# Kernel tuning notes

Measured on AMD Instinct MI355X. Metric: run time of the kernel, lower is better.

Reference implementation:

```python
import jax, jax.numpy as jnp
import numpy as np

NUM_E = 50000
EMBED_DIM = 128
HID_DIM = 200
B = 512
N = 50  # candidate_num / history length
ITER_NUM = 3
ALPHA = 0.5
WEIGHT_BASE = 1.0
SQUASH_W = 1.0
SQUASH_EPS = 1e-9
L2_EPS = 1e-12  # torch F.normalize default eps


def setup_inputs() -> dict:
    key = jax.random.key(0)
    k1, k2, k3, k4, k5, k6, k7 = jax.random.split(key, 7)
    idx = jax.random.randint(k1, (B, N), 0, NUM_E)
    times = jax.random.randint(k2, (B, N), 0, 365)
    # embeddings: normal then row-wise L2 normalize (as in init_embeddings)
    emb = jax.random.normal(k3, (NUM_E, EMBED_DIM), dtype=jnp.float32)
    embeddings = emb / jnp.maximum(jnp.linalg.norm(emb, axis=1, keepdims=True), L2_EPS)
    Ws_w = jax.random.normal(k4, (HID_DIM, EMBED_DIM), dtype=jnp.float32) * (2.0 / (HID_DIM + EMBED_DIM)) ** 0.5
    Ws_b = jnp.zeros((HID_DIM,), dtype=jnp.float32)
    mlp_w = jax.random.normal(k5, (NUM_E, HID_DIM), dtype=jnp.float32) * (2.0 / (NUM_E + HID_DIM)) ** 0.5
    mlp_b = jnp.zeros((NUM_E,), dtype=jnp.float32)
    return {"idx": idx, "times": times, "embeddings": embeddings,
            "Ws_w": Ws_w, "Ws_b": Ws_b, "mlp_w": mlp_w, "mlp_b": mlp_b}


def _squash(s):
    # s: [B, H]; squash over last axis (original axis=-2 on [B,1,1,H,1])
    sq = jnp.sum(s * s, axis=-1, keepdims=True)
    scale = sq / (SQUASH_W + sq) / jnp.sqrt(sq + SQUASH_EPS)
    return scale * s


def reference(idx, times, embeddings, Ws_w, Ws_b, mlp_w, mlp_b):
    # gather history embeddings: [B, N, D]
    embeds = embeddings[idx]
    # temporal weighting -> initial routing logits b_ij: [B, N]
    b = (WEIGHT_BASE + 1.0) / (WEIGHT_BASE + times.astype(jnp.float32))
    # Ws linear (dropout is identity at eval): [B, N, H]
    x = jnp.einsum('bnd,hd->bnh', embeds, Ws_w) + Ws_b
    # u_hat: L2-normalized over H
    u_hat = x / jnp.maximum(jnp.linalg.norm(x, axis=-1, keepdims=True), L2_EPS)
    u_det = jax.lax.stop_gradient(u_hat)
    # dynamic routing, fixed ITER_NUM iterations
    for r in range(ITER_NUM):
        c = jax.nn.softmax(b, axis=1) * N            # [B, N]
        s = jnp.einsum('bn,bnh->bh', c, u_hat)       # [B, H]
        v = _squash(s)                               # [B, H]
        if r < ITER_NUM - 1:
            b = b + jnp.einsum('bnh,bh->bn', u_det, v)
    poses, c_ij = v, c                               # [B, H], [B, N]
    # p_ij: scatter-add c_ij per entity id (math of one_hot^T @ c_ij)
    p = jnp.zeros((B, NUM_E), dtype=jnp.float32)
    p = p.at[jnp.arange(B)[:, None], idx].add(c_ij)
    p = jax.nn.softmax(p, axis=1)
    # decoder mlp (reflect=False)
    scores = poses @ mlp_w.T + mlp_b                 # [B, NUM_E]
    sims = jax.nn.softmax(scores, axis=1)
    return jnp.log(ALPHA * p + (1.0 - ALPHA) * sims)
```

## Files before the change

kernel.cpp:

```cpp
#include <hip/hip_runtime.h>
#include <stdint.h>

#define NUM_E 50000
#define EMBED_DIM 128
#define HID_DIM 200
#define BATCH 512
#define NN 50
#define KPAD 224
#define NKT 7
#define NTT2 3136
#define NXB 196
#define PACK_UNITS 784
#define USTRIDE 201

typedef short s16x8 __attribute__((ext_vector_type(8)));
typedef float f32x4 __attribute__((ext_vector_type(4)));

__device__ inline unsigned short f2bf(float f) {
  union { float f; unsigned u; } v; v.f = f;
  unsigned r = v.u + 0x7FFF + ((v.u >> 16) & 1);
  return (unsigned short)(r >> 16);
}
__device__ inline float bf2f(unsigned short b) {
  union { unsigned u; float f; } v; v.u = ((unsigned)b) << 16;
  return v.f;
}

__device__ __forceinline__ void gl_lds16(const unsigned short* g, unsigned short* l) {
  __builtin_amdgcn_global_load_lds(
      (const __attribute__((address_space(1))) unsigned int*)g,
      (__attribute__((address_space(3))) unsigned int*)l, 16, 0, 0);
}

template<int PASS>
__device__ __forceinline__ void gemm_tile(
    int yb, int xb, char* buf, int tid,
    const unsigned short* Ap, const unsigned short* Bp, const float* mlp_b,
    const float* D_ws, float* S_ws, float* out)
{
  unsigned short* Bs = (unsigned short*)buf;
  float* red = (float*)(buf + 16384);
  const int w = tid >> 6, lane = tid & 63;
  const int q = lane >> 4, l15 = lane & 15;
  const int mt0 = yb * 4;
  const int m0 = yb * 64;
  const int ntb = xb * 16 + w * 4;

  if (PASS == 1 && tid < 64) {
    red[tid]      = 0.5f / D_ws[m0 + tid];
    red[64 + tid] = 0.5f / S_ws[m0 + tid];
  }
  float bias[4];
  #pragma unroll
  for (int nl = 0; nl < 4; ++nl) {
    const int col = (ntb + nl) * 16 + l15;
    bias[nl] = (col < NUM_E) ? mlp_b[col] : 0.f;
  }
  const unsigned short* apBase = Ap + (size_t)mt0 * NKT * 512;

  f32x4 acc[4][4];
  #pragma unroll
  for (int i = 0; i < 4; i++)
    #pragma unroll
    for (int j = 0; j < 4; j++) acc[i][j] = (f32x4){0, 0, 0, 0};

  for (int kt = 0; kt < NKT; ++kt) {
    #pragma unroll
    for (int nl = 0; nl < 4; ++nl)
      gl_lds16(Bp + ((size_t)(ntb + nl) * NKT + kt) * 512 + lane * 8,
               &Bs[(w * 4 + nl) * 512]);
    s16x8 a[4];
    #pragma unroll
    for (int mi = 0; mi < 4; ++mi)
      a[mi] = *(const s16x8*)&apBase[((mi * NKT + kt) * 64 + lane) * 8];
    __syncthreads();
    s16x8 bfr[4];
    #pragma unroll
    for (int nl = 0; nl < 4; ++nl)
      bfr[nl] = *(const s16x8*)&Bs[((w * 4 + nl) * 64 + lane) * 8];
    #pragma unroll
    for (int nl = 0; nl < 4; ++nl)
      #pragma unroll
      for (int mi = 0; mi < 4; ++mi)
        acc[mi][nl] = __builtin_amdgcn_mfma_f32_16x16x32_bf16(a[mi], bfr[nl], acc[mi][nl], 0, 0, 0);
    __syncthreads();
  }

  if (PASS == 0) {
    float rs[4][4];
    #pragma unroll
    for (int mi = 0; mi < 4; mi++)
      #pragma unroll
      for (int p = 0; p < 4; p++) rs[mi][p] = 0.f;
    #pragma unroll
    for (int mi = 0; mi < 4; ++mi)
      #pragma unroll
      for (int nl = 0; nl < 4; ++nl) {
        const int col = (ntb + nl) * 16 + l15;
        #pragma unroll
        for (int p = 0; p < 4; p++) {
          const float v = acc[mi][nl][p] + bias[nl];
          rs[mi][p] += (col < NUM_E) ? __expf(v) : 0.f;
        }
      }
    #pragma unroll
    for (int m = 1; m < 16; m <<= 1)
      for (int mi = 0; mi < 4; mi++)
        for (int p = 0; p < 4; p++)
          rs[mi][p] += __shfl_xor(rs[mi][p], m, 64);
    if (l15 == 0)
      for (int mi = 0; mi < 4; mi++)
        for (int p = 0; p < 4; p++)
          red[w * 64 + mi * 16 + q * 4 + p] = rs[mi][p];
    __syncthreads();
    if (tid < 64)
      atomicAdd(&S_ws[m0 + tid],
                red[tid] + red[64 + tid] + red[128 + tid] + red[192 + tid]);
  } else {
    #pragma unroll
    for (int mi = 0; mi < 4; ++mi) {
      #pragma unroll
      for (int p = 0; p < 4; p++) {
        const int rl = mi * 16 + q * 4 + p;
        const float invD = red[rl];
        const float invS = red[64 + rl];
        const int row = m0 + rl;
        #pragma unroll
        for (int nl = 0; nl < 4; ++nl) {
          const int col = (ntb + nl) * 16 + l15;
          if (col < NUM_E) {
            const float v = acc[mi][nl][p] + bias[nl];
            out[(size_t)row * NUM_E + col] = __logf(fmaf(__expf(v), invS, invD));
          }
        }
      }
    }
  }
}

__global__ __launch_bounds__(256, 3) void k_stage1(
    const int* __restrict__ idx, const int* __restrict__ times,
    const float* __restrict__ emb, const float* __restrict__ Ws_w,
    const float* __restrict__ Ws_b, const float* __restrict__ mlp_w,
    unsigned short* __restrict__ Bp, unsigned short* __restrict__ Ap,
    float* __restrict__ poses_f, float* __restrict__ expa_ws,
    float* __restrict__ D_ws, float* __restrict__ S_ws)
{
  __shared__ __align__(16) char buf[40320];
  __shared__ float cc[NN], bb[NN], vv[HID_DIM], red4[4], scaleS;
  __shared__ int sidx[NN];
  const int u = blockIdx.x;
  const int tid = threadIdx.x;
  const int w = tid >> 6, lane = tid & 63;
  const int q = lane >> 4, l15 = lane & 15;

  if (u < BATCH) {
    const int b = u;
    if (tid < NN) {
      sidx[tid] = idx[b * NN + tid];
      bb[tid] = 2.0f / (1.0f + (float)times[b * NN + tid]);
    }
    __syncthreads();
    unsigned short* Afr = (unsigned short*)buf;
    unsigned short* Bfr = (unsigned short*)(buf + 16384);
    for (int v = tid; v < 1024; v += 256) {
      const int row = v >> 4, c = v & 15;
      const int kt = c >> 2, qq = c & 3;
      unsigned short tmp[8] __attribute__((aligned(16)));
      if (row < NN) {
        const float* src = emb + (size_t)sidx[row] * EMBED_DIM + c * 8;
        float4 f0 = *(const float4*)src;
        float4 f1 = *(const float4*)(src + 4);
        tmp[0] = f2bf(f0.x); tmp[1] = f2bf(f0.y); tmp[2] = f2bf(f0.z); tmp[3] = f2bf(f0.w);
        tmp[4] = f2bf(f1.x); tmp[5] = f2bf(f1.y); tmp[6] = f2bf(f1.z); tmp[7] = f2bf(f1.w);
      } else {
        for (int j = 0; j < 8; j++) tmp[j] = 0;
      }
      *(uint4*)&Afr[(((row >> 4) * 4 + kt) * 64 + qq * 16 + (row & 15)) * 8] = *(uint4*)tmp;
    }
    f32x4 acc[4][4];
    #pragma unroll
    for (int i = 0; i < 4; i++)
      #pragma unroll
      for (int j = 0; j < 4; j++) acc[i][j] = (f32x4){0, 0, 0, 0};
    __syncthreads();
    for (int kt = 0; kt < 4; ++kt) {
      for (int v = tid; v < 832; v += 256) {
        const int n = v >> 2, cq = v & 3;
        unsigned short tmp[8] __attribute__((aligned(16)));
        if (n < HID_DIM) {
          const float* src = Ws_w + (size_t)n * EMBED_DIM + kt * 32 + cq * 8;
          float4 f0 = *(const float4*)src;
          float4 f1 = *(const float4*)(src + 4);
          tmp[0] = f2bf(f0.x); tmp[1] = f2bf(f0.y); tmp[2] = f2bf(f0.z); tmp[3] = f2bf(f0.w);
          tmp[4] = f2bf(f1.x); tmp[5] = f2bf(f1.y); tmp[6] = f2bf(f1.z); tmp[7] = f2bf(f1.w);
        } else {
          for (int j = 0; j < 8; j++) tmp[j] = 0;
        }
        *(uint4*)&Bfr[((n >> 4) * 64 + cq * 16 + (n & 15)) * 8] = *(uint4*)tmp;
      }
      __syncthreads();
      s16x8 a[4];
      #pragma unroll
      for (int mt = 0; mt < 4; ++mt)
        a[mt] = *(const s16x8*)&Afr[((mt * 4 + kt) * 64 + lane) * 8];
      #pragma unroll
      for (int ii = 0; ii < 4; ++ii) {
        const int nt = w + ii * 4;
        if (nt < 13) {
          s16x8 bv = *(const s16x8*)&Bfr[(nt * 64 + lane) * 8];
          #pragma unroll
          for (int mt = 0; mt < 4; ++mt)
            acc[mt][ii] = __builtin_amdgcn_mfma_f32_16x16x32_bf16(a[mt], bv, acc[mt][ii], 0, 0, 0);
        }
      }
      __syncthreads();
    }
    float* uu = (float*)buf;
    #pragma unroll
    for (int ii = 0; ii < 4; ++ii) {
      const int nt = w + ii * 4;
      if (nt < 13) {
        const int col = nt * 16 + l15;
        if (col < HID_DIM) {
          const float bv = Ws_b[col];
          #pragma unroll
          for (int mt = 0; mt < 4; ++mt)
            #pragma unroll
            for (int p = 0; p < 4; p++) {
              const int row = mt * 16 + q * 4 + p;
              if (row < NN) uu[row * USTRIDE + col] = acc[mt][ii][p] + bv;
            }
        }
      }
    }
    __syncthreads();
    const int un = tid >> 2, uc0 = (tid & 3) * 50;
    if (un < NN) {
      float s = 0.f;
      for (int j = 0; j < 50; j++) {
        const float x = uu[un * USTRIDE + uc0 + j];
        s += x * x;
      }
      s += __shfl_xor(s, 1, 64);
      s += __shfl_xor(s, 2, 64);
      const float inv = 1.0f / fmaxf(sqrtf(s), 1e-12f);
      for (int j = 0; j < 50; j++) uu[un * USTRIDE + uc0 + j] *= inv;
    }
    __syncthreads();
    for (int it = 0; it < 3; ++it) {
      if (tid < 64) {
        float x = (tid < NN) ? bb[tid] : -1e30f;
        float m = x;
        for (int d = 1; d < 64; d <<= 1) m = fmaxf(m, __shfl_xor(m, d, 64));
        float e = (tid < NN) ? __expf(x - m) : 0.f;
        float s = e;
        for (int d = 1; d < 64; d <<= 1) s += __shfl_xor(s, d, 64);
        if (tid < NN) cc[tid] = e * (float)NN / s;
      }
      __syncthreads();
      float sh = 0.f;
      if (tid < HID_DIM)
        for (int n = 0; n < NN; n++) sh += cc[n] * uu[n * USTRIDE + tid];
      float sq2 = (tid < HID_DIM) ? sh * sh : 0.f;
      for (int d = 1; d < 64; d <<= 1) sq2 += __shfl_xor(sq2, d, 64);
      if ((tid & 63) == 0) red4[tid >> 6] = sq2;
      __syncthreads();
      if (tid == 0) {
        const float t2 = red4[0] + red4[1] + red4[2] + red4[3];
        scaleS = t2 / (1.0f + t2) / sqrtf(t2 + 1e-9f);
      }
      __syncthreads();
      if (tid < HID_DIM) vv[tid] = scaleS * sh;
      __syncthreads();
      if (it < 2) {
        float d = 0.f;
        if (un < NN)
          for (int j = 0; j < 50; j++)
            d += uu[un * USTRIDE + uc0 + j] * vv[uc0 + j];
        d += __shfl_xor(d, 1, 64);
        d += __shfl_xor(d, 2, 64);
        if (un < NN && (tid & 3) == 0) bb[un] += d;
        __syncthreads();
      }
    }
    if (tid < KPAD) {
      const float val = (tid < HID_DIM) ? vv[tid] : 0.f;
      const int kt = tid >> 5, rem = tid & 31, qq = rem >> 3, j = rem & 7;
      const int mt = b >> 4, ll = b & 15;
      Ap[(size_t)(((mt * NKT + kt) * 64) + qq * 16 + ll) * 8 + j] = f2bf(val);
    }
    if (tid < HID_DIM) poses_f[b * HID_DIM + tid] = vv[tid];
    if (tid < 64) {
      float a2 = 0.f; int first = 1;
      const int my = (tid < NN) ? sidx[tid] : -1;
      if (tid < NN) {
        for (int n = 0; n < NN; n++)
          if (sidx[n] == my) { a2 += cc[n]; if (n < tid) first = 0; }
        expa_ws[b * NN + tid] = __expf(a2);
      }
      float contrib = (tid < NN && first) ? (__expf(a2) - 1.0f) : 0.f;
      for (int d = 1; d < 64; d <<= 1) contrib += __shfl_xor(contrib, d, 64);
      if (tid == 0) D_ws[b] = (float)NUM_E + contrib;
    }
  } else if (u < BATCH + PACK_UNITS) {
    const int pb = u - BATCH;
    unsigned short* smem = (unsigned short*)buf;
    const size_t base_f = (size_t)pb * 64 * HID_DIM;
    const float4* src4 = (const float4*)(mlp_w + base_f);
    for (int i = tid; i < 3200; i += 256) {
      float4 f;
      if (base_f + 4 * (size_t)i + 4 <= (size_t)NUM_E * HID_DIM) f = src4[i];
      else f = make_float4(0.f, 0.f, 0.f, 0.f);
      unsigned short t4[4] __attribute__((aligned(8))) = {
        f2bf(f.x), f2bf(f.y), f2bf(f.z), f2bf(f.w)};
      *(uint2*)&smem[i * 4] = *(uint2*)t4;
    }
    __syncthreads();
    const int nt0 = pb * 4;
    unsigned short* dst = Bp + (size_t)nt0 * NKT * 512;
    for (int s2 = 0; s2 < 7; ++s2) {
      const int fi = s2 * 256 + tid;
      const int fr = fi >> 6;
      const int ln = fi & 63;
      const int nt_l = fr / 7, kt = fr - nt_l * 7;
      const int r = nt_l * 16 + (ln & 15);
      const int kb = kt * 32 + (ln >> 4) * 8;
      uint4 val;
      if (kb < HID_DIM) val = *(const uint4*)&smem[r * HID_DIM + kb];
      else val = make_uint4(0, 0, 0, 0);
      *(uint4*)&dst[(size_t)fi * 8] = val;
    }
  } else {
    S_ws[tid] = 0.f;
    S_ws[256 + tid] = 0.f;
  }
}

template<int PASS>
__global__ __launch_bounds__(256, 4) void k_gemm(
    const unsigned short* __restrict__ Ap, const unsigned short* __restrict__ Bp,
    const float* __restrict__ mlp_b, const float* __restrict__ D_ws,
    float* __restrict__ S_ws, float* __restrict__ out)
{
  __shared__ __align__(16) char buf2[17408];
  const int id = blockIdx.x;
  const int yb = id / 200;
  const int xb = id - yb * 200;
  if (xb >= NXB) return;
  gemm_tile<PASS>(yb, xb, buf2, threadIdx.x, Ap, Bp, mlp_b, D_ws, S_ws, out);
}

__global__ __launch_bounds__(256) void k_fix(
    const int* __restrict__ idx, const float* __restrict__ expa,
    const float* __restrict__ poses_f, const float* __restrict__ mlp_w,
    const float* __restrict__ mlp_b, const float* __restrict__ D_ws,
    const float* __restrict__ S_ws, float* __restrict__ out)
{
  const int t = blockIdx.x * 4 + (threadIdx.x >> 6);
  const int lane = threadIdx.x & 63;
  if (t >= BATCH * NN) return;
  const int b = t / NN;
  const int j = idx[t];
  float dot = 0.f;
  for (int h = lane; h < HID_DIM; h += 64)
    dot += poses_f[b * HID_DIM + h] * mlp_w[(size_t)j * HID_DIM + h];
  for (int m = 1; m < 64; m <<= 1) dot += __shfl_xor(dot, m, 64);
  if (lane == 0) {
    const float s = dot + mlp_b[j];
    out[(size_t)b * NUM_E + j] = __logf(0.5f * expa[t] / D_ws[b] +
                                        0.5f * __expf(s) / S_ws[b]);
  }
}

extern "C" void kernel_launch(void* const* d_in, const int* in_sizes, int n_in,
                              void* d_out, int out_size, void* d_ws, size_t ws_size,
                              hipStream_t stream) {
  const int*   idx   = (const int*)d_in[0];
  const int*   times = (const int*)d_in[1];
  const float* emb   = (const float*)d_in[2];
  const float* Ws_w  = (const float*)d_in[3];
  const float* Ws_b  = (const float*)d_in[4];
  const float* mlp_w = (const float*)d_in[5];
  const float* mlp_b = (const float*)d_in[6];
  float* out = (float*)d_out;

  char* ws = (char*)d_ws;
  unsigned short* Bp    = (unsigned short*)ws; ws += (size_t)NTT2 * NKT * 64 * 8 * 2;
  unsigned short* Ap    = (unsigned short*)ws; ws += (size_t)32 * NKT * 64 * 8 * 2;
  float* poses_f        = (float*)ws;          ws += (size_t)BATCH * HID_DIM * 4;
  float* expa           = (float*)ws;          ws += (size_t)BATCH * NN * 4;
  float* D_ws           = (float*)ws;          ws += (size_t)BATCH * 4;
  float* S_ws           = (float*)ws;          ws += (size_t)BATCH * 4;

  k_stage1 <<<dim3(BATCH + PACK_UNITS + 1), 256, 0, stream>>>(
      idx, times, emb, Ws_w, Ws_b, mlp_w, Bp, Ap, poses_f, expa, D_ws, S_ws);
  k_gemm<0><<<dim3(1600),           256, 0, stream>>>(Ap, Bp, mlp_b, D_ws, S_ws, out);
  k_gemm<1><<<dim3(1600),           256, 0, stream>>>(Ap, Bp, mlp_b, D_ws, S_ws, out);
  k_fix    <<<dim3(BATCH * NN / 4), 256, 0, stream>>>(idx, expa, poses_f, mlp_w, mlp_b, D_ws, S_ws, out);
}
```

Before: 257.2 us.

## Stash bf16 scores instead of recomputing GEMM in second softmax pass

Replaces the two-pass recompute scheme (GEMM once for row sums, GEMM again for output) with a single GEMM pass that writes bf16-rounded logits to a workspace stash while accumulating exp sums, followed by an elementwise kernel that reads the stash and writes the log-mixture output. This removes the second GEMM but adds about 51 MB of bf16 stash writes and reads. The stash writes are scattered 2-byte stores in MFMA layout, which may coalesce poorly, and rounding logits to bf16 adds precision loss.

```diff
diff --git a/kernel.cpp b/kernel.cpp
--- a/kernel.cpp
+++ b/kernel.cpp
@@ -32,24 +32,26 @@
       (__attribute__((address_space(3))) unsigned int*)l, 16, 0, 0);
 }
 
-template<int PASS>
-__device__ __forceinline__ void gemm_tile(
-    int yb, int xb, char* buf, int tid,
-    const unsigned short* Ap, const unsigned short* Bp, const float* mlp_b,
-    const float* D_ws, float* S_ws, float* out)
+__global__ __launch_bounds__(256, 4) void k_score(
+    const unsigned short* __restrict__ Ap, const unsigned short* __restrict__ Bp,
+    const float* __restrict__ mlp_b, unsigned short* __restrict__ stash,
+    float* __restrict__ S_ws)
 {
+  __shared__ __align__(16) char buf[17408];
+  const int id = blockIdx.x;
+  const int yb = id / 200;
+  const int xb = id - yb * 200;
+  if (xb >= NXB) return;
+
   unsigned short* Bs = (unsigned short*)buf;
   float* red = (float*)(buf + 16384);
+  const int tid = threadIdx.x;
   const int w = tid >> 6, lane = tid & 63;
   const int q = lane >> 4, l15 = lane & 15;
   const int mt0 = yb * 4;
   const int m0 = yb * 64;
   const int ntb = xb * 16 + w * 4;
 
-  if (PASS == 1 && tid < 64) {
-    red[tid]      = 0.5f / D_ws[m0 + tid];
-    red[64 + tid] = 0.5f / S_ws[m0 + tid];
-  }
   float bias[4];
   #pragma unroll
   for (int nl = 0; nl < 4; ++nl) {
@@ -86,55 +88,68 @@
     __syncthreads();
   }
 
-  if (PASS == 0) {
-    float rs[4][4];
-    #pragma unroll
-    for (int mi = 0; mi < 4; mi++)
-      #pragma unroll
-      for (int p = 0; p < 4; p++) rs[mi][p] = 0.f;
-    #pragma unroll
-    for (int mi = 0; mi < 4; ++mi)
-      #pragma unroll
-      for (int nl = 0; nl < 4; ++nl) {
-        const int col = (ntb + nl) * 16 + l15;
-        #pragma unroll
-        for (int p = 0; p < 4; p++) {
-          const float v = acc[mi][nl][p] + bias[nl];
-          rs[mi][p] += (col < NUM_E) ? __expf(v) : 0.f;
-        }
-      }
-    #pragma unroll
-    for (int m = 1; m < 16; m <<= 1)
-      for (int mi = 0; mi < 4; mi++)
-        for (int p = 0; p < 4; p++)
-          rs[mi][p] += __shfl_xor(rs[mi][p], m, 64);
-    if (l15 == 0)
-      for (int mi = 0; mi < 4; mi++)
-        for (int p = 0; p < 4; p++)
-          red[w * 64 + mi * 16 + q * 4 + p] = rs[mi][p];
-    __syncthreads();
-    if (tid < 64)
-      atomicAdd(&S_ws[m0 + tid],
-                red[tid] + red[64 + tid] + red[128 + tid] + red[192 + tid]);
-  } else {
-    #pragma unroll
-    for (int mi = 0; mi < 4; ++mi) {
+  float rs[4][4];
+  #pragma unroll
+  for (int mi = 0; mi < 4; mi++)
+    #pragma unroll
+    for (int p = 0; p < 4; p++) rs[mi][p] = 0.f;
+  #pragma unroll
+  for (int mi = 0; mi < 4; ++mi)
+    #pragma unroll
+    for (int nl = 0; nl < 4; ++nl) {
+      const int col = (ntb + nl) * 16 + l15;
       #pragma unroll
       for (int p = 0; p < 4; p++) {
-        const int rl = mi * 16 + q * 4 + p;
-        const float invD = red[rl];
-        const float invS = red[64 + rl];
-        const int row = m0 + rl;
-        #pragma unroll
-        for (int nl = 0; nl < 4; ++nl) {
-          const int col = (ntb + nl) * 16 + l15;
-          if (col < NUM_E) {
-            const float v = acc[mi][nl][p] + bias[nl];
-            out[(size_t)row * NUM_E + col] = __logf(fmaf(__expf(v), invS, invD));
-          }
+        if (col < NUM_E) {
+          const float v = acc[mi][nl][p] + bias[nl];
+          const unsigned short vb = f2bf(v);
+          const int row = m0 + mi * 16 + q * 4 + p;
+          stash[(size_t)row * NUM_E + col] = vb;
+          rs[mi][p] += __expf(bf2f(vb));
         }
       }
     }
+  #pragma unroll
+  for (int m = 1; m < 16; m <<= 1)
+    for (int mi = 0; mi < 4; mi++)
+      for (int p = 0; p < 4; p++)
+        rs[mi][p] += __shfl_xor(rs[mi][p], m, 64);
+  if (l15 == 0)
+    for (int mi = 0; mi < 4; mi++)
+      for (int p = 0; p < 4; p++)
+        red[w * 64 + mi * 16 + q * 4 + p] = rs[mi][p];
+  __syncthreads();
+  if (tid < 64)
+    atomicAdd(&S_ws[m0 + tid],
+              red[tid] + red[64 + tid] + red[128 + tid] + red[192 + tid]);
+}
+
+__global__ __launch_bounds__(256) void k_final(
+    const unsigned short* __restrict__ stash,
+    const float* __restrict__ D_ws, const float* __restrict__ S_ws,
+    float* __restrict__ out)
+{
+  const int COLS8 = NUM_E / 8;
+  const int total = BATCH * COLS8;
+  const int stride = gridDim.x * 256;
+  for (int u = blockIdx.x * 256 + threadIdx.x; u < total; u += stride) {
+    const int b = u / COLS8;
+    const int c8 = u - b * COLS8;
+    const float invD = 0.5f / D_ws[b];
+    const float invS = 0.5f / S_ws[b];
+    const size_t base = (size_t)b * NUM_E + (size_t)c8 * 8;
+    const uint4 raw = *(const uint4*)(stash + base);
+    float o[8];
+    const unsigned wds[4] = {raw.x, raw.y, raw.z, raw.w};
+    #pragma unroll
+    for (int j = 0; j < 4; ++j) {
+      const float v0 = bf2f((unsigned short)(wds[j] & 0xFFFF));
+      const float v1 = bf2f((unsigned short)(wds[j] >> 16));
+      o[2 * j]     = __logf(fmaf(__expf(v0), invS, invD));
+      o[2 * j + 1] = __logf(fmaf(__expf(v1), invS, invD));
+    }
+    *(float4*)(out + base)     = make_float4(o[0], o[1], o[2], o[3]);
+    *(float4*)(out + base + 4) = make_float4(o[4], o[5], o[6], o[7]);
   }
 }
 
@@ -335,20 +350,6 @@
     S_ws[tid] = 0.f;
     S_ws[256 + tid] = 0.f;
   }
-}
-
-template<int PASS>
-__global__ __launch_bounds__(256, 4) void k_gemm(
-    const unsigned short* __restrict__ Ap, const unsigned short* __restrict__ Bp,
-    const float* __restrict__ mlp_b, const float* __restrict__ D_ws,
-    float* __restrict__ S_ws, float* __restrict__ out)
-{
-  __shared__ __align__(16) char buf2[17408];
-  const int id = blockIdx.x;
-  const int yb = id / 200;
-  const int xb = id - yb * 200;
-  if (xb >= NXB) return;
-  gemm_tile<PASS>(yb, xb, buf2, threadIdx.x, Ap, Bp, mlp_b, D_ws, S_ws, out);
 }
 
 __global__ __launch_bounds__(256) void k_fix(
@@ -392,10 +393,11 @@
   float* expa           = (float*)ws;          ws += (size_t)BATCH * NN * 4;
   float* D_ws           = (float*)ws;          ws += (size_t)BATCH * 4;
   float* S_ws           = (float*)ws;          ws += (size_t)BATCH * 4;
+  unsigned short* stash = (unsigned short*)ws; ws += (size_t)BATCH * NUM_E * 2;
 
   k_stage1 <<<dim3(BATCH + PACK_UNITS + 1), 256, 0, stream>>>(
       idx, times, emb, Ws_w, Ws_b, mlp_w, Bp, Ap, poses_f, expa, D_ws, S_ws);
-  k_gemm<0><<<dim3(1600),           256, 0, stream>>>(Ap, Bp, mlp_b, D_ws, S_ws, out);
-  k_gemm<1><<<dim3(1600),           256, 0, stream>>>(Ap, Bp, mlp_b, D_ws, S_ws, out);
+  k_score  <<<dim3(1600), 256, 0, stream>>>(Ap, Bp, mlp_b, stash, S_ws);
+  k_final  <<<dim3(2048), 256, 0, stream>>>(stash, D_ws, S_ws, out);
   k_fix    <<<dim3(BATCH * NN / 4), 256, 0, stream>>>(idx, expa, poses_f, mlp_w, mlp_b, D_ws, S_ws, out);
 }
```

Result: slower. 265.2 us (+3.1%).
